# Optimization experiments

Measured on AMD Instinct MI355X. Metric: run time of the kernel, lower is better.

Reference implementation:

```python
import jax, jax.numpy as jnp
import numpy as np

B, P, Q, E, H, VOCAB = 32, 512, 64, 300, 256, 50000
HH = H // 2  # per-direction GRU hidden size
NEG = -1e7


def setup_inputs() -> dict:
    key = jax.random.key(0)
    ks = list(jax.random.split(key, 32))
    def nk():
        return ks.pop()
    def tokens(kk, kl, T):
        t = jax.random.randint(kk, (B, T), 1, VOCAB)
        lens = jax.random.randint(kl, (B,), T // 2, T + 1)
        m = jnp.arange(T)[None, :] < lens[:, None]
        return jnp.where(m, t, 0)  # 0 is the padding index
    passage = tokens(nk(), nk(), P)
    question = tokens(nk(), nk(), Q)
    emb = jax.random.normal(nk(), (VOCAB, E), jnp.float32) * 0.1
    emb = emb.at[0].set(0.0)  # padding row
    kg = 1.0 / np.sqrt(HH)
    def U(shape):
        return jax.random.uniform(nk(), shape, jnp.float32, -kg, kg)
    inp = {"passage": passage, "question": question, "emb": emb}
    for pre in ("p", "q"):
        for d in ("f", "b"):
            inp[pre + "_wih_" + d] = U((3 * HH, E))
            inp[pre + "_whh_" + d] = U((3 * HH, HH))
            inp[pre + "_bih_" + d] = U((3 * HH,))
            inp[pre + "_bhh_" + d] = U((3 * HH,))
    kl = 1.0 / np.sqrt(3 * H)
    def UL(shape):
        return jax.random.uniform(nk(), shape, jnp.float32, -kl, kl)
    inp["attn_w"] = UL((3 * H,)); inp["attn_b"] = UL(())
    inp["start_w"] = UL((3 * H,)); inp["start_b"] = UL(())
    inp["end_w"] = UL((3 * H,)); inp["end_b"] = UL(())
    return inp


def gru_dir(x, mask, wih, whh, bih, bhh, reverse):
    # x: (B,T,E), mask: (B,T) bool. Masked steps freeze h and emit 0,
    # matching pack_padded/pad_packed semantics.
    xp = jnp.einsum('bte,he->bth', x, wih) + bih  # (B,T,3*HH)
    def step(h, inp):
        xt, mt = inp  # (B,3*HH), (B,1)
        hp = h @ whh.T + bhh
        xr, xz, xn = jnp.split(xt, 3, axis=-1)
        hr, hz, hn = jnp.split(hp, 3, axis=-1)
        r = jax.nn.sigmoid(xr + hr)
        z = jax.nn.sigmoid(xz + hz)
        n = jnp.tanh(xn + r * hn)
        hnew = (1.0 - z) * n + z * h
        hnew = jnp.where(mt, hnew, h)
        return hnew, jnp.where(mt, hnew, 0.0)
    h0 = jnp.zeros((x.shape[0], HH), x.dtype)
    xs = (jnp.swapaxes(xp, 0, 1), jnp.swapaxes(mask[:, :, None], 0, 1))
    _, ys = jax.lax.scan(step, h0, xs, reverse=reverse)
    return jnp.swapaxes(ys, 0, 1)  # (B,T,HH)


def bigru(x, mask, wih_f, whh_f, bih_f, bhh_f, wih_b, whh_b, bih_b, bhh_b):
    f = gru_dir(x, mask, wih_f, whh_f, bih_f, bhh_f, False)
    b = gru_dir(x, mask, wih_b, whh_b, bih_b, bhh_b, True)
    return jnp.concatenate([f, b], axis=-1)  # (B,T,H)


def reference(passage, question, emb,
              p_wih_f, p_whh_f, p_bih_f, p_bhh_f,
              p_wih_b, p_whh_b, p_bih_b, p_bhh_b,
              q_wih_f, q_whh_f, q_bih_f, q_bhh_f,
              q_wih_b, q_whh_b, q_bih_b, q_bhh_b,
              attn_w, attn_b, start_w, start_b, end_w, end_b):
    pm = passage != 0
    qm = question != 0
    ep = emb[passage]  # (B,P,E)
    eq = emb[question]  # (B,Q,E)
    penc = bigru(ep, pm, p_wih_f, p_whh_f, p_bih_f, p_bhh_f,
                 p_wih_b, p_whh_b, p_bih_b, p_bhh_b)  # (B,P,H)
    qenc = bigru(eq, qm, q_wih_f, q_whh_f, q_bih_f, q_bhh_f,
                 q_wih_b, q_whh_b, q_bih_b, q_bhh_b)  # (B,Q,H)
    # Decomposed BiDAF-style co-attention: Linear([p; q; p*q]) -> 1 is
    # w1.p + w2.q + (p*w3).q + b  (same math, no (B,P,Q,3H) tensor).
    w1, w2, w3 = jnp.split(attn_w, 3)
    logits = (penc @ w1)[:, :, None] + (qenc @ w2)[:, None, :] \
        + jnp.einsum('bph,bqh->bpq', penc * w3, qenc) + attn_b  # (B,P,Q)
    probs = jax.nn.softmax(jnp.where(qm[:, None, :], logits, NEG), axis=-1)
    attw = jnp.einsum('bpq,bqh->bph', probs, qenc)  # (B,P,H)
    comb = jnp.concatenate([penc, attw, penc * attw], axis=-1)  # (B,P,3H)
    start = jnp.where(pm, comb @ start_w + start_b, NEG)
    end = jnp.where(pm, comb @ end_w + end_b, NEG)
    return (start, end,
            jax.nn.log_softmax(start, axis=-1),
            jax.nn.log_softmax(end, axis=-1))
```

## Files before the change

kernel.cpp:

```cpp
#include <hip/hip_runtime.h>
#include <hip/hip_bf16.h>

#define B_ 32
#define P_ 512
#define Q_ 64
#define E_ 300
#define KP 320
#define H_ 256
#define HH_ 128
#define NEG (-1e7f)
#define BP (B_*P_)
#define BQ (B_*Q_)

typedef __attribute__((ext_vector_type(8))) short bf16x8;
typedef __attribute__((ext_vector_type(4))) float f32x4;
typedef _Float16 half2v __attribute__((ext_vector_type(2)));
typedef unsigned int u32;

__device__ __hip_bfloat16 g_ep[BP][KP];
__device__ __hip_bfloat16 g_eq[BQ][KP];
__device__ __hip_bfloat16 g_wp[768][KP];
__device__ __hip_bfloat16 g_wq[768][KP];
__device__ float g_biasp[768];
__device__ float g_biasq[768];
__device__ float g_biasn[4][HH_];
__device__ uint4 g_whhw[4*512*12];
__device__ float g_xtp[2L*P_*B_*384];
__device__ float g_xtq[2L*Q_*B_*384];
__device__ float g_penc[BP*H_];
__device__ float g_qenc[BQ*H_];

struct PrepArgs { const float* wih[4]; const float* bih[4]; const float* bhh[4]; };

__global__ __launch_bounds__(64) void k_prepw(PrepArgs pa) {
    int r = blockIdx.x;
    int pq = r / 768, col = r % 768;
    int dir = col / 384, within = col % 384, gate = within / 128;
    int idx = pq * 2 + dir;
    const float* wsrc = pa.wih[idx] + within * E_;
    __hip_bfloat16* dst = pq ? g_wq[col] : g_wp[col];
    for (int c = threadIdx.x; c < KP; c += 64)
        dst[c] = __float2bfloat16(c < E_ ? wsrc[c] : 0.f);
    if (threadIdx.x == 0) {
        float bsum = pa.bih[idx][within] + (gate < 2 ? pa.bhh[idx][within] : 0.f);
        (pq ? g_biasq : g_biasp)[col] = bsum;
        if (within >= 256) g_biasn[idx][within - 256] = pa.bhh[idx][within];
    }
}

__global__ __launch_bounds__(512) void k_prepw2(const float* w0, const float* w1,
                                               const float* w2, const float* w3) {
    int widx = blockIdx.x;
    const float* whh = widx == 0 ? w0 : widx == 1 ? w1 : widx == 2 ? w2 : w3;
    int tid = threadIdx.x;
    int j = tid >> 2, q = tid & 3;
    uint4* dst = g_whhw + ((long)widx * 512 + tid) * 12;
    for (int g = 0; g < 3; g++)
        for (int i = 0; i < 4; i++) {
            const float* src = whh + (long)(g * 128 + j) * HH_ + q * 32 + i * 8;
            u32 p[4];
            #pragma unroll
            for (int e = 0; e < 4; e++) {
                half2v hp;
                hp[0] = (_Float16)src[2 * e];
                hp[1] = (_Float16)src[2 * e + 1];
                p[e] = __builtin_bit_cast(u32, hp);
            }
            dst[g * 4 + i] = make_uint4(p[0], p[1], p[2], p[3]);
        }
}

__global__ __launch_bounds__(256) void k_gather(const int* pass, const int* ques, const float* emb) {
    int row = blockIdx.x * 4 + (threadIdx.x >> 6);
    int lane = threadIdx.x & 63;
    const int* tsrc; __hip_bfloat16* dst; int r, T;
    if (row < BP) { r = row; tsrc = pass; dst = &g_ep[r][0]; T = P_; }
    else          { r = row - BP; tsrc = ques; dst = &g_eq[r][0]; T = Q_; }
    int b = r & 31, t = r >> 5;
    int tk = tsrc[b * T + t];
    const float* src = emb + (long)tk * E_;
    #pragma unroll
    for (int i = 0; i < 5; i++) {
        int c = i * 64 + lane;
        float v = (c < E_) ? src[c] : 0.f;
        dst[c] = __float2bfloat16(v);
    }
}

__global__ __launch_bounds__(256) void k_gemm() {
    int bx = blockIdx.x;
    int isQ = bx >= 128;
    int mblk = isQ ? bx - 128 : bx;
    const __hip_bfloat16* A  = isQ ? &g_eq[0][0] : &g_ep[0][0];
    const __hip_bfloat16* Bw = isQ ? &g_wq[0][0] : &g_wp[0][0];
    const float* bias = isQ ? g_biasq : g_biasp;
    float* Xt = isQ ? g_xtq : g_xtp;
    const int T = isQ ? Q_ : P_;
    __shared__ __hip_bfloat16 As[128][40];
    __shared__ __hip_bfloat16 Bs[128][40];
    int m0 = mblk * 128, n0 = blockIdx.y * 128;
    int tid = threadIdx.x, lane = tid & 63, w = tid >> 6;
    int wm = (w & 1) * 64, wn = (w >> 1) * 64;
    f32x4 acc[4][4] = {};
    int lr = tid >> 1, lc = (tid & 1) * 16;
    for (int kt = 0; kt < KP; kt += 32) {
        *(bf16x8*)&As[lr][lc]   = *(const bf16x8*)&A [(m0 + lr) * KP + kt + lc];
        *(bf16x8*)&As[lr][lc+8] = *(const bf16x8*)&A [(m0 + lr) * KP + kt + lc + 8];
        *(bf16x8*)&Bs[lr][lc]   = *(const bf16x8*)&Bw[(n0 + lr) * KP + kt + lc];
        *(bf16x8*)&Bs[lr][lc+8] = *(const bf16x8*)&Bw[(n0 + lr) * KP + kt + lc + 8];
        __syncthreads();
        int kb = (lane >> 4) * 8, l15 = lane & 15;
        bf16x8 af[4], bfr[4];
        #pragma unroll
        for (int i = 0; i < 4; i++) af[i]  = *(bf16x8*)&As[wm + i*16 + l15][kb];
        #pragma unroll
        for (int j = 0; j < 4; j++) bfr[j] = *(bf16x8*)&Bs[wn + j*16 + l15][kb];
        #pragma unroll
        for (int i = 0; i < 4; i++)
            #pragma unroll
            for (int j = 0; j < 4; j++)
                acc[i][j] = __builtin_amdgcn_mfma_f32_16x16x32_bf16(af[i], bfr[j], acc[i][j], 0, 0, 0);
        __syncthreads();
    }
    int l15 = lane & 15, lr4 = (lane >> 4) * 4;
    #pragma unroll
    for (int jj = 0; jj < 4; jj++) {
        int n = n0 + wn + jj * 16 + l15;
        float bn = bias[n];
        int dirn = n >= 384;
        int col = n - dirn * 384;
        float* Cx = Xt + (long)dirn * T * B_ * 384;
        #pragma unroll
        for (int i = 0; i < 4; i++) {
            int mb = m0 + wm + i * 16 + lr4;
            int t = mb >> 5, bb = mb & 31;
            #pragma unroll
            for (int q = 0; q < 4; q++)
                Cx[((long)t * B_ + bb + q) * 384 + col] = acc[i][jj][q] + bn;
        }
    }
}

__global__ __launch_bounds__(256) void k_maskz(const int* pass, const int* ques) {
    int tid = threadIdx.x;
    for (int row = blockIdx.x; row < BP + BQ; row += 256) {
        int isQ = row >= BP;
        int rr = isQ ? row - BP : row;
        int T = isQ ? Q_ : P_;
        int tkn = isQ ? ques[rr] : pass[rr];
        if (tkn == 0) {
            int b = rr / T, t = rr % T;
            float* xt = isQ ? g_xtq : g_xtp;
            int dir = tid >> 7, col = tid & 127;
            xt[((long)dir * T * B_ + (long)t * B_ + b) * 384 + 128 + col] = 1e9f;
        }
    }
}

#define D1(A, WU, HU) A = __builtin_amdgcn_fdot2( \
    __builtin_bit_cast(half2v, (WU)), __builtin_bit_cast(half2v, (HU)), A, false);
#define D4(A, W, H) D1(A,(W).x,(H).x) D1(A,(W).y,(H).y) D1(A,(W).z,(H).z) D1(A,(W).w,(H).w)

__global__ __launch_bounds__(512, 1) void k_gru() {
    int blk = blockIdx.x;
    int isQ = blk >> 6, loc = blk & 63, dir = loc >> 5, b = loc & 31;
    const int T = isQ ? Q_ : P_;
    const float* xt = (isQ ? g_xtq : g_xtp) + (long)dir * T * B_ * 384;
    float* outp = isQ ? g_qenc : g_penc;
    int widx = isQ * 2 + dir;
    int tid = threadIdx.x;
    int j = tid >> 2, q = tid & 3;
    const uint4* wp = g_whhw + ((long)widx * 512 + tid) * 12;
    uint4 w00 = wp[0], w01 = wp[1], w02 = wp[2],  w03 = wp[3];
    uint4 w10 = wp[4], w11 = wp[5], w12 = wp[6],  w13 = wp[7];
    uint4 w20 = wp[8], w21 = wp[9], w22 = wp[10], w23 = wp[11];
    float bnn = g_biasn[widx][j];
    __shared__ uint hbuf[2][64];
    int t0 = dir ? T - 1 : 0;
    int sdt = dir ? -(B_ * 384) : (B_ * 384);
    int sdo = dir ? -H_ : H_;
    int off = (t0 * B_ + b) * 384 + j;
    int ooff = (b * T + t0) * H_ + dir * HH_ + j;
    float xr = xt[off], xz = xt[off + 128], xn = xt[off + 256];
    uint4 z4 = {0u, 0u, 0u, 0u};
    uint4 h0 = z4, h1 = z4, h2 = z4, h3 = z4;
    float hold = 0.f;
    for (int st = 0; st < T; st++) {
        int offn = off + ((st + 1 < T) ? sdt : 0);
        float nxr = xt[offn], nxz = xt[offn + 128], nxn = xt[offn + 256];
        float ar0 = 0.f, ar1 = 0.f, az0 = 0.f, az1 = 0.f, an0 = 0.f, an1 = 0.f;
        D4(ar0, w00, h0) D4(ar1, w01, h1) D4(ar0, w02, h2) D4(ar1, w03, h3)
        D4(az0, w10, h0) D4(az1, w11, h1) D4(az0, w12, h2) D4(az1, w13, h3)
        D4(an0, w20, h0) D4(an1, w21, h1) D4(an0, w22, h2) D4(an1, w23, h3)
        float ar = ar0 + ar1, az = az0 + az1, an = an0 + an1;
        ar += __shfl_xor(ar, 1); ar += __shfl_xor(ar, 2);
        az += __shfl_xor(az, 1); az += __shfl_xor(az, 2);
        an += __shfl_xor(an, 1); an += __shfl_xor(an, 2);
        float rg = __builtin_amdgcn_rcpf(1.f + __expf(-(ar + xr)));
        float zg = __builtin_amdgcn_rcpf(1.f + __expf(-(az + xz)));
        float ta = __builtin_amdgcn_fmed3f(fmaf(rg, an + bnn, xn), -15.f, 15.f);
        float e2 = __expf(2.f * ta);
        float th = fmaf(-2.f, __builtin_amdgcn_rcpf(e2 + 1.f), 1.f);
        float hv = fmaf(zg, hold - th, th);
        hold = hv;
        if (q == 0) {
            outp[ooff] = hv;
            ((_Float16*)hbuf[st & 1])[j] = (_Float16)hv;
        }
        asm volatile("s_waitcnt lgkmcnt(0)\n\ts_barrier" ::: "memory");
        const uint4* hb = (const uint4*)hbuf[st & 1] + q * 4;
        h0 = hb[0]; h1 = hb[1]; h2 = hb[2]; h3 = hb[3];
        off = offn; ooff += sdo;
        xr = nxr; xz = nxz; xn = nxn;
    }
}

#define QH 288
__global__ __launch_bounds__(256) void k_attn(const int* pass, const int* ques,
        const float* attn_w, const float* attn_b, const float* start_w,
        const float* start_b, const float* end_w, const float* end_b, float* out) {
    __shared__ _Float16 qsh[64][QH];
    __shared__ uint pw3u[4][128];
    __shared__ _Float16 w2h[256];
    int b = blockIdx.x >> 4, pblk = blockIdx.x & 15;
    int tid = threadIdx.x, lane = tid & 63, wid = tid >> 6;
    {
        int q = tid >> 2, hb = (tid & 3) * 64;
        const float* src = g_qenc + ((long)(b * Q_ + q)) * H_ + hb;
        #pragma unroll
        for (int i = 0; i < 16; i++) {
            float4 v = *(const float4*)(src + i * 4);
            half2v a, c;
            a[0] = (_Float16)v.x; a[1] = (_Float16)v.y;
            c[0] = (_Float16)v.z; c[1] = (_Float16)v.w;
            uint2 pk = { __builtin_bit_cast(u32, a), __builtin_bit_cast(u32, c) };
            *(uint2*)&qsh[q][hb + i * 4] = pk;
        }
        if (tid < 128) {
            half2v a;
            a[0] = (_Float16)attn_w[256 + 2 * tid];
            a[1] = (_Float16)attn_w[256 + 2 * tid + 1];
            *(uint*)&w2h[2 * tid] = __builtin_bit_cast(u32, a);
        }
    }
    __syncthreads();
    int qm = ques[b * Q_ + lane] != 0;
    float s2;
    {
        float a0 = 0.f, a1 = 0.f;
        const uint4* qrow = (const uint4*)&qsh[lane][0];
        const uint4* wrow = (const uint4*)w2h;
        #pragma unroll
        for (int i = 0; i < 32; i++) {
            uint4 qv = qrow[i]; uint4 wv = wrow[i];
            D1(a0, qv.x, wv.x) D1(a1, qv.y, wv.y) D1(a0, qv.z, wv.z) D1(a1, qv.w, wv.w)
        }
        s2 = a0 + a1;
    }
    float4 w1 = *(const float4*)(attn_w + 4 * lane);
    float4 w3 = *(const float4*)(attn_w + 512 + 4 * lane);
    float4 sA = *(const float4*)(start_w + 4 * lane);
    float4 sB = *(const float4*)(start_w + 256 + 4 * lane);
    float4 sC = *(const float4*)(start_w + 512 + 4 * lane);
    float4 eA = *(const float4*)(end_w + 4 * lane);
    float4 eB = *(const float4*)(end_w + 256 + 4 * lane);
    float4 eC = *(const float4*)(end_w + 512 + 4 * lane);
    float ab = attn_b[0], sb = start_b[0], ebv = end_b[0];
    uint* mypw = pw3u[wid];
    const uint4* pwrow = (const uint4*)mypw;
    for (int r = 0; r < 8; r++) {
        int p = pblk * 32 + wid * 8 + r;
        long prow = (long)(b * P_ + p);
        int ptok = pass[prow];
        float4 pv = *(const float4*)(g_penc + prow * H_ + 4 * lane);
        float s1p = pv.x * w1.x + pv.y * w1.y + pv.z * w1.z + pv.w * w1.w;
        #pragma unroll
        for (int s = 1; s < 64; s <<= 1) s1p += __shfl_xor(s1p, s);
        half2v h01, h23;
        h01[0] = (_Float16)(pv.x * w3.x); h01[1] = (_Float16)(pv.y * w3.y);
        h23[0] = (_Float16)(pv.z * w3.z); h23[1] = (_Float16)(pv.w * w3.w);
        mypw[2 * lane]     = __builtin_bit_cast(u32, h01);
        mypw[2 * lane + 1] = __builtin_bit_cast(u32, h23);
        asm volatile("s_waitcnt lgkmcnt(0)" ::: "memory");
        float c0 = 0.f, c1 = 0.f;
        const uint4* qrow = (const uint4*)&qsh[lane][0];
        #pragma unroll
        for (int i = 0; i < 32; i++) {
            uint4 qv = qrow[i]; uint4 wv = pwrow[i];
            D1(c0, qv.x, wv.x) D1(c1, qv.y, wv.y) D1(c0, qv.z, wv.z) D1(c1, qv.w, wv.w)
        }
        float logit = qm ? (s1p + s2 + c0 + c1 + ab) : NEG;
        float m = logit;
        #pragma unroll
        for (int s = 1; s < 64; s <<= 1) m = fmaxf(m, __shfl_xor(m, s));
        float e = __expf(logit - m);
        float ss = e;
        #pragma unroll
        for (int s = 1; s < 64; s <<= 1) ss += __shfl_xor(ss, s);
        float prob = e / ss;
        half2v aw01 = {(_Float16)0.f, (_Float16)0.f}, aw23 = aw01;
        #pragma unroll 8
        for (int q2 = 0; q2 < 64; q2++) {
            float pq = __shfl(prob, q2);
            half2v ph; ph[0] = (_Float16)pq; ph[1] = ph[0];
            uint2 qv = *(const uint2*)&qsh[q2][4 * lane];
            aw01 += __builtin_bit_cast(half2v, qv.x) * ph;
            aw23 += __builtin_bit_cast(half2v, qv.y) * ph;
        }
        float a0 = (float)aw01[0], a1 = (float)aw01[1];
        float a2 = (float)aw23[0], a3 = (float)aw23[1];
        float spv = pv.x * sA.x + a0 * sB.x + pv.x * a0 * sC.x
                  + pv.y * sA.y + a1 * sB.y + pv.y * a1 * sC.y
                  + pv.z * sA.z + a2 * sB.z + pv.z * a2 * sC.z
                  + pv.w * sA.w + a3 * sB.w + pv.w * a3 * sC.w;
        float epv = pv.x * eA.x + a0 * eB.x + pv.x * a0 * eC.x
                  + pv.y * eA.y + a1 * eB.y + pv.y * a1 * eC.y
                  + pv.z * eA.z + a2 * eB.z + pv.z * a2 * eC.z
                  + pv.w * eA.w + a3 * eB.w + pv.w * a3 * eC.w;
        #pragma unroll
        for (int s = 1; s < 64; s <<= 1) {
            spv += __shfl_xor(spv, s);
            epv += __shfl_xor(epv, s);
        }
        if (lane == 0) {
            int pm = (ptok != 0);
            out[prow]      = pm ? (spv + sb)  : NEG;
            out[BP + prow] = pm ? (epv + ebv) : NEG;
        }
    }
}

__global__ __launch_bounds__(256) void k_lsm(float* out) {
    int b = blockIdx.x >> 1, which = blockIdx.x & 1;
    const float* src = out + which * BP + b * P_;
    int tid = threadIdx.x;
    float v0 = src[tid], v1 = src[tid + 256];
    __shared__ float red[4];
    float m = fmaxf(v0, v1);
    #pragma unroll
    for (int s = 1; s < 64; s <<= 1) m = fmaxf(m, __shfl_xor(m, s));
    if ((tid & 63) == 0) red[tid >> 6] = m;
    __syncthreads();
    m = fmaxf(fmaxf(red[0], red[1]), fmaxf(red[2], red[3]));
    __syncthreads();
    float ss = __expf(v0 - m) + __expf(v1 - m);
    #pragma unroll
    for (int s = 1; s < 64; s <<= 1) ss += __shfl_xor(ss, s);
    if ((tid & 63) == 0) red[tid >> 6] = ss;
    __syncthreads();
    float lse = m + logf(red[0] + red[1] + red[2] + red[3]);
    float* dst = out + (2 + which) * BP + b * P_;
    dst[tid] = v0 - lse;
    dst[tid + 256] = v1 - lse;
}

extern "C" void kernel_launch(void* const* d_in, const int* in_sizes, int n_in,
                              void* d_out, int out_size, void* d_ws, size_t ws_size,
                              hipStream_t stream) {
    const int* pass = (const int*)d_in[0];
    const int* ques = (const int*)d_in[1];
    const float* emb = (const float*)d_in[2];
    PrepArgs pa;
    const float* whh[4];
    const int base[4] = {3, 7, 11, 15};
    for (int i = 0; i < 4; i++) {
        pa.wih[i] = (const float*)d_in[base[i] + 0];
        whh[i]    = (const float*)d_in[base[i] + 1];
        pa.bih[i] = (const float*)d_in[base[i] + 2];
        pa.bhh[i] = (const float*)d_in[base[i] + 3];
    }
    const float* attn_w  = (const float*)d_in[19];
    const float* attn_b  = (const float*)d_in[20];
    const float* start_w = (const float*)d_in[21];
    const float* start_b = (const float*)d_in[22];
    const float* end_w   = (const float*)d_in[23];
    const float* end_b   = (const float*)d_in[24];
    float* out = (float*)d_out;

    k_prepw <<<dim3(1536), dim3(64), 0, stream>>>(pa);
    k_prepw2<<<dim3(4), dim3(512), 0, stream>>>(whh[0], whh[1], whh[2], whh[3]);
    k_gather<<<dim3((BP + BQ) / 4), dim3(256), 0, stream>>>(pass, ques, emb);
    k_gemm  <<<dim3(144, 6), dim3(256), 0, stream>>>();
    k_maskz <<<dim3(256), dim3(256), 0, stream>>>(pass, ques);
    k_gru   <<<dim3(128), dim3(512), 0, stream>>>();
    k_attn  <<<dim3(B_ * 16), dim3(256), 0, stream>>>(pass, ques, attn_w, attn_b,
                                                      start_w, start_b, end_w, end_b, out);
    k_lsm   <<<dim3(64), dim3(256), 0, stream>>>(out);
}
```

Measured before the change: 432.5 us.

## Fuse embedding gather and masking into GEMM, store gate preactivations as fp16

Merges the two weight-prep kernels into one launch. The embedding gather moves into the GEMM's A-tile load, so the bf16 staging copy of the embeddings is no longer written and re-read. The padding mask (z-gate forced to +inf) is now applied in the GEMM epilogue, which removes the separate mask kernel. The input-projection buffer is stored as fp16 instead of fp32, halving GEMM write and GRU read traffic. The costs are uncoalesced fp32 gather reads repeated across all six N-blocks, and fp16 range and precision limits on the preactivations.

```diff
diff --git a/kernel.cpp b/kernel.cpp
--- a/kernel.cpp
+++ b/kernel.cpp
@@ -17,95 +17,92 @@
 typedef _Float16 half2v __attribute__((ext_vector_type(2)));
 typedef unsigned int u32;
 
-__device__ __hip_bfloat16 g_ep[BP][KP];
-__device__ __hip_bfloat16 g_eq[BQ][KP];
 __device__ __hip_bfloat16 g_wp[768][KP];
 __device__ __hip_bfloat16 g_wq[768][KP];
 __device__ float g_biasp[768];
 __device__ float g_biasq[768];
 __device__ float g_biasn[4][HH_];
 __device__ uint4 g_whhw[4*512*12];
-__device__ float g_xtp[2L*P_*B_*384];
-__device__ float g_xtq[2L*Q_*B_*384];
+__device__ _Float16 g_xtp[2L*P_*B_*384];
+__device__ _Float16 g_xtq[2L*Q_*B_*384];
 __device__ float g_penc[BP*H_];
 __device__ float g_qenc[BQ*H_];
 
-struct PrepArgs { const float* wih[4]; const float* bih[4]; const float* bhh[4]; };
-
-__global__ __launch_bounds__(64) void k_prepw(PrepArgs pa) {
-    int r = blockIdx.x;
-    int pq = r / 768, col = r % 768;
-    int dir = col / 384, within = col % 384, gate = within / 128;
-    int idx = pq * 2 + dir;
-    const float* wsrc = pa.wih[idx] + within * E_;
-    __hip_bfloat16* dst = pq ? g_wq[col] : g_wp[col];
-    for (int c = threadIdx.x; c < KP; c += 64)
-        dst[c] = __float2bfloat16(c < E_ ? wsrc[c] : 0.f);
-    if (threadIdx.x == 0) {
-        float bsum = pa.bih[idx][within] + (gate < 2 ? pa.bhh[idx][within] : 0.f);
-        (pq ? g_biasq : g_biasp)[col] = bsum;
-        if (within >= 256) g_biasn[idx][within - 256] = pa.bhh[idx][within];
-    }
-}
-
-__global__ __launch_bounds__(512) void k_prepw2(const float* w0, const float* w1,
-                                               const float* w2, const float* w3) {
-    int widx = blockIdx.x;
-    const float* whh = widx == 0 ? w0 : widx == 1 ? w1 : widx == 2 ? w2 : w3;
+struct PrepArgs { const float* wih[4]; const float* whh[4]; const float* bih[4]; const float* bhh[4]; };
+
+__global__ __launch_bounds__(512) void k_prep(PrepArgs pa) {
+    int blk = blockIdx.x;
     int tid = threadIdx.x;
-    int j = tid >> 2, q = tid & 3;
-    uint4* dst = g_whhw + ((long)widx * 512 + tid) * 12;
-    for (int g = 0; g < 3; g++)
-        for (int i = 0; i < 4; i++) {
-            const float* src = whh + (long)(g * 128 + j) * HH_ + q * 32 + i * 8;
-            u32 p[4];
-            #pragma unroll
-            for (int e = 0; e < 4; e++) {
-                half2v hp;
-                hp[0] = (_Float16)src[2 * e];
-                hp[1] = (_Float16)src[2 * e + 1];
-                p[e] = __builtin_bit_cast(u32, hp);
+    if (blk < 192) {
+        int r = blk * 8 + (tid >> 6);
+        int lane = tid & 63;
+        int pq = r / 768, col = r % 768;
+        int dir = col / 384, within = col % 384, gate = within / 128;
+        int idx = pq * 2 + dir;
+        const float* wsrc = pa.wih[idx] + within * E_;
+        __hip_bfloat16* dst = pq ? g_wq[col] : g_wp[col];
+        for (int c = lane; c < KP; c += 64)
+            dst[c] = __float2bfloat16(c < E_ ? wsrc[c] : 0.f);
+        if (lane == 0) {
+            float bsum = pa.bih[idx][within] + (gate < 2 ? pa.bhh[idx][within] : 0.f);
+            (pq ? g_biasq : g_biasp)[col] = bsum;
+            if (within >= 256) g_biasn[idx][within - 256] = pa.bhh[idx][within];
+        }
+    } else {
+        int widx = blk - 192;
+        const float* whh = pa.whh[widx];
+        int j = tid >> 2, q = tid & 3;
+        uint4* dst = g_whhw + ((long)widx * 512 + tid) * 12;
+        for (int g = 0; g < 3; g++)
+            for (int i = 0; i < 4; i++) {
+                const float* src = whh + (long)(g * 128 + j) * HH_ + q * 32 + i * 8;
+                u32 p[4];
+                #pragma unroll
+                for (int e = 0; e < 4; e++) {
+                    half2v hp;
+                    hp[0] = (_Float16)src[2 * e];
+                    hp[1] = (_Float16)src[2 * e + 1];
+                    p[e] = __builtin_bit_cast(u32, hp);
+                }
+                dst[g * 4 + i] = make_uint4(p[0], p[1], p[2], p[3]);
             }
-            dst[g * 4 + i] = make_uint4(p[0], p[1], p[2], p[3]);
-        }
-}
-
-__global__ __launch_bounds__(256) void k_gather(const int* pass, const int* ques, const float* emb) {
-    int row = blockIdx.x * 4 + (threadIdx.x >> 6);
-    int lane = threadIdx.x & 63;
-    const int* tsrc; __hip_bfloat16* dst; int r, T;
-    if (row < BP) { r = row; tsrc = pass; dst = &g_ep[r][0]; T = P_; }
-    else          { r = row - BP; tsrc = ques; dst = &g_eq[r][0]; T = Q_; }
-    int b = r & 31, t = r >> 5;
-    int tk = tsrc[b * T + t];
-    const float* src = emb + (long)tk * E_;
-    #pragma unroll
-    for (int i = 0; i < 5; i++) {
-        int c = i * 64 + lane;
-        float v = (c < E_) ? src[c] : 0.f;
-        dst[c] = __float2bfloat16(v);
-    }
-}
-
-__global__ __launch_bounds__(256) void k_gemm() {
+    }
+}
+
+__global__ __launch_bounds__(256) void k_gemm(const int* pass, const int* ques, const float* emb) {
     int bx = blockIdx.x;
     int isQ = bx >= 128;
     int mblk = isQ ? bx - 128 : bx;
-    const __hip_bfloat16* A  = isQ ? &g_eq[0][0] : &g_ep[0][0];
     const __hip_bfloat16* Bw = isQ ? &g_wq[0][0] : &g_wp[0][0];
     const float* bias = isQ ? g_biasq : g_biasp;
-    float* Xt = isQ ? g_xtq : g_xtp;
+    _Float16* Xt = isQ ? g_xtq : g_xtp;
+    const int* tsrc = isQ ? ques : pass;
     const int T = isQ ? Q_ : P_;
     __shared__ __hip_bfloat16 As[128][40];
     __shared__ __hip_bfloat16 Bs[128][40];
+    __shared__ int toks[128];
     int m0 = mblk * 128, n0 = blockIdx.y * 128;
     int tid = threadIdx.x, lane = tid & 63, w = tid >> 6;
     int wm = (w & 1) * 64, wn = (w >> 1) * 64;
+    if (tid < 128) {
+        int m = m0 + tid;
+        int t = m >> 5, bb = m & 31;
+        toks[tid] = tsrc[bb * T + t];
+    }
     f32x4 acc[4][4] = {};
     int lr = tid >> 1, lc = (tid & 1) * 16;
+    __syncthreads();
+    long arow = (long)toks[lr] * E_;
     for (int kt = 0; kt < KP; kt += 32) {
-        *(bf16x8*)&As[lr][lc]   = *(const bf16x8*)&A [(m0 + lr) * KP + kt + lc];
-        *(bf16x8*)&As[lr][lc+8] = *(const bf16x8*)&A [(m0 + lr) * KP + kt + lc + 8];
+        const float* er = emb + arow + kt + lc;
+        __hip_bfloat16 a16[16];
+        #pragma unroll
+        for (int i = 0; i < 16; i++) {
+            int c = kt + lc + i;
+            a16[i] = __float2bfloat16((c < E_) ? er[i] : 0.f);
+        }
+        *(bf16x8*)&As[lr][lc]   = *(bf16x8*)&a16[0];
+        *(bf16x8*)&As[lr][lc+8] = *(bf16x8*)&a16[8];
         *(bf16x8*)&Bs[lr][lc]   = *(const bf16x8*)&Bw[(n0 + lr) * KP + kt + lc];
         *(bf16x8*)&Bs[lr][lc+8] = *(const bf16x8*)&Bw[(n0 + lr) * KP + kt + lc + 8];
         __syncthreads();
@@ -123,36 +120,26 @@
         __syncthreads();
     }
     int l15 = lane & 15, lr4 = (lane >> 4) * 4;
+    const _Float16 inf16 = __builtin_bit_cast(_Float16, (unsigned short)0x7C00);
     #pragma unroll
     for (int jj = 0; jj < 4; jj++) {
         int n = n0 + wn + jj * 16 + l15;
         float bn = bias[n];
         int dirn = n >= 384;
         int col = n - dirn * 384;
-        float* Cx = Xt + (long)dirn * T * B_ * 384;
+        int zcol = (col >= 128) & (col < 256);
+        _Float16* Cx = Xt + (long)dirn * T * B_ * 384;
         #pragma unroll
         for (int i = 0; i < 4; i++) {
             int mb = m0 + wm + i * 16 + lr4;
             int t = mb >> 5, bb = mb & 31;
+            int lrow = wm + i * 16 + lr4;
             #pragma unroll
-            for (int q = 0; q < 4; q++)
-                Cx[((long)t * B_ + bb + q) * 384 + col] = acc[i][jj][q] + bn;
-        }
-    }
-}
-
-__global__ __launch_bounds__(256) void k_maskz(const int* pass, const int* ques) {
-    int tid = threadIdx.x;
-    for (int row = blockIdx.x; row < BP + BQ; row += 256) {
-        int isQ = row >= BP;
-        int rr = isQ ? row - BP : row;
-        int T = isQ ? Q_ : P_;
-        int tkn = isQ ? ques[rr] : pass[rr];
-        if (tkn == 0) {
-            int b = rr / T, t = rr % T;
-            float* xt = isQ ? g_xtq : g_xtp;
-            int dir = tid >> 7, col = tid & 127;
-            xt[((long)dir * T * B_ + (long)t * B_ + b) * 384 + 128 + col] = 1e9f;
+            for (int q = 0; q < 4; q++) {
+                _Float16 v = (_Float16)(acc[i][jj][q] + bn);
+                if (zcol && toks[lrow + q] == 0) v = inf16;
+                Cx[((long)t * B_ + bb + q) * 384 + col] = v;
+            }
         }
     }
 }
@@ -165,7 +152,7 @@
     int blk = blockIdx.x;
     int isQ = blk >> 6, loc = blk & 63, dir = loc >> 5, b = loc & 31;
     const int T = isQ ? Q_ : P_;
-    const float* xt = (isQ ? g_xtq : g_xtp) + (long)dir * T * B_ * 384;
+    const _Float16* xt = (isQ ? g_xtq : g_xtp) + (long)dir * T * B_ * 384;
     float* outp = isQ ? g_qenc : g_penc;
     int widx = isQ * 2 + dir;
     int tid = threadIdx.x;
@@ -181,13 +168,13 @@
     int sdo = dir ? -H_ : H_;
     int off = (t0 * B_ + b) * 384 + j;
     int ooff = (b * T + t0) * H_ + dir * HH_ + j;
-    float xr = xt[off], xz = xt[off + 128], xn = xt[off + 256];
+    float xr = (float)xt[off], xz = (float)xt[off + 128], xn = (float)xt[off + 256];
     uint4 z4 = {0u, 0u, 0u, 0u};
     uint4 h0 = z4, h1 = z4, h2 = z4, h3 = z4;
     float hold = 0.f;
     for (int st = 0; st < T; st++) {
         int offn = off + ((st + 1 < T) ? sdt : 0);
-        float nxr = xt[offn], nxz = xt[offn + 128], nxn = xt[offn + 256];
+        float nxr = (float)xt[offn], nxz = (float)xt[offn + 128], nxn = (float)xt[offn + 256];
         float ar0 = 0.f, ar1 = 0.f, az0 = 0.f, az1 = 0.f, an0 = 0.f, an1 = 0.f;
         D4(ar0, w00, h0) D4(ar1, w01, h1) D4(ar0, w02, h2) D4(ar1, w03, h3)
         D4(az0, w10, h0) D4(az1, w11, h1) D4(az0, w12, h2) D4(az1, w13, h3)
@@ -361,11 +348,10 @@
     const int* ques = (const int*)d_in[1];
     const float* emb = (const float*)d_in[2];
     PrepArgs pa;
-    const float* whh[4];
     const int base[4] = {3, 7, 11, 15};
     for (int i = 0; i < 4; i++) {
         pa.wih[i] = (const float*)d_in[base[i] + 0];
-        whh[i]    = (const float*)d_in[base[i] + 1];
+        pa.whh[i] = (const float*)d_in[base[i] + 1];
         pa.bih[i] = (const float*)d_in[base[i] + 2];
         pa.bhh[i] = (const float*)d_in[base[i] + 3];
     }
@@ -377,13 +363,10 @@
     const float* end_b   = (const float*)d_in[24];
     float* out = (float*)d_out;
 
-    k_prepw <<<dim3(1536), dim3(64), 0, stream>>>(pa);
-    k_prepw2<<<dim3(4), dim3(512), 0, stream>>>(whh[0], whh[1], whh[2], whh[3]);
-    k_gather<<<dim3((BP + BQ) / 4), dim3(256), 0, stream>>>(pass, ques, emb);
-    k_gemm  <<<dim3(144, 6), dim3(256), 0, stream>>>();
-    k_maskz <<<dim3(256), dim3(256), 0, stream>>>(pass, ques);
-    k_gru   <<<dim3(128), dim3(512), 0, stream>>>();
-    k_attn  <<<dim3(B_ * 16), dim3(256), 0, stream>>>(pass, ques, attn_w, attn_b,
-                                                      start_w, start_b, end_w, end_b, out);
-    k_lsm   <<<dim3(64), dim3(256), 0, stream>>>(out);
-}
+    k_prep <<<dim3(196), dim3(512), 0, stream>>>(pa);
+    k_gemm <<<dim3(144, 6), dim3(256), 0, stream>>>(pass, ques, emb);
+    k_gru  <<<dim3(128), dim3(512), 0, stream>>>();
+    k_attn <<<dim3(B_ * 16), dim3(256), 0, stream>>>(pass, ques, attn_w, attn_b,
+                                                     start_w, start_b, end_w, end_b, out);
+    k_lsm  <<<dim3(64), dim3(256), 0, stream>>>(out);
+}
```

New measurement: 393.8 us. 9.0% less time.
